# Kernel tuning notes

Hardware: AMD Instinct MI355X
Metric: run time of the kernel (lower is better)

The kernel has to match this reference:

```python
import jax, jax.numpy as jnp
import numpy as np

B, T, K = 256, 512, 128          # batch, seq_len, n_tag
START, STOP = 126, 127           # tag2idx[START_TAG], tag2idx[STOP_TAG]
NEG = -10000.0                   # same constant the torch module uses


def setup_inputs() -> dict:
    key = jax.random.key(0)
    k1, k2, k3 = jax.random.split(key, 3)
    feats = jax.random.normal(k1, (B, T, K), dtype=jnp.float32)
    tags = jax.random.randint(k2, (B, T), 0, 126)  # never START/STOP
    # learned CRF transition matrix: trans[to, from]
    transitions = 0.1 * jax.random.normal(k3, (K, K), dtype=jnp.float32)
    transitions = transitions.at[START, :].set(NEG).at[:, STOP].set(NEG)
    return {"feats": feats, "tags": tags, "transitions": transitions}


def _forward_alg(feats, trans):
    """Batched CRF forward algorithm. feats [B,T,K] -> log Z [B]."""
    b = feats.shape[0]
    init = jnp.full((b, K), NEG, feats.dtype).at[:, START].set(0.0)

    def step(alpha, feat_t):
        # scores[b, to, from] = alpha[b, from] + trans[to, from]
        scores = alpha[:, None, :] + trans[None, :, :]
        alpha_new = jax.nn.logsumexp(scores, axis=-1) + feat_t
        return alpha_new, None

    alpha, _ = jax.lax.scan(step, init, jnp.swapaxes(feats, 0, 1))
    return jax.nn.logsumexp(alpha + trans[STOP][None, :], axis=-1)


def _score_sentence(feats, tags, trans):
    """Batched gold path score. feats [B,T,K], tags [B,T] -> [B]."""
    b = feats.shape[0]
    start_col = jnp.full((b, 1), START, tags.dtype)
    tags_ext = jnp.concatenate([start_col, tags], axis=1)      # [B,T+1]
    trans_sc = trans[tags_ext[:, 1:], tags_ext[:, :-1]].sum(axis=1)
    emit_sc = jnp.take_along_axis(feats, tags[..., None], axis=2)[..., 0].sum(axis=1)
    return trans_sc + emit_sc + trans[STOP, tags[:, -1]]


def _viterbi(feats, trans):
    """Batched Viterbi decode. Returns (path_score [B], path [B,T])."""
    b = feats.shape[0]
    init = jnp.full((b, K), NEG, feats.dtype).at[:, START].set(0.0)

    def step(alpha, feat_t):
        scores = alpha[:, None, :] + trans[None, :, :]   # [B,to,from]
        bptr = jnp.argmax(scores, axis=-1)               # [B,to]
        alpha_new = jnp.max(scores, axis=-1) + feat_t
        return alpha_new, bptr

    alpha, bptrs = jax.lax.scan(step, init, jnp.swapaxes(feats, 0, 1))
    term = alpha + trans[STOP][None, :]
    last_tag = jnp.argmax(term, axis=-1)                 # [B]
    path_score = jnp.max(term, axis=-1)

    def back(tag_t, bp_t):
        prev = jnp.take_along_axis(bp_t, tag_t[:, None], axis=1)[:, 0]
        return prev, tag_t

    _, path = jax.lax.scan(back, last_tag, bptrs, reverse=True)  # [T,B]
    return path_score, jnp.swapaxes(path, 0, 1)


def reference(feats, tags, transitions):
    log_z = _forward_alg(feats, transitions)             # forward_alg per sentence
    gold = _score_sentence(feats, tags, transitions)     # score_sentence
    path_score, pred = _viterbi(feats, transitions)      # viterbi_decode
    loss = jnp.sum(log_z - gold) / jnp.float32(feats.shape[0] * feats.shape[1])
    return loss, path_score, pred
```

## Files before the change

kernel.cpp:

```cpp
#include <hip/hip_runtime.h>
#include <cstdint>
#include <cstddef>

#define BB 256
#define TT 512
#define KK 128
#define START_TAG 126
#define STOP_TAG 127
#define NEGV (-10000.0f)
#define NINF (-__builtin_huge_valf())

template<int CTRL>
__device__ __forceinline__ float dppf(float v, float old) {
  return __int_as_float(__builtin_amdgcn_update_dpp(
      __float_as_int(old), __float_as_int(v), CTRL, 0xf, 0xf, false));
}
template<int CTRL>
__device__ __forceinline__ int dppi(int v, int old) {
  return __builtin_amdgcn_update_dpp(old, v, CTRL, 0xf, 0xf, false);
}
__device__ __forceinline__ float wave_max63(float x) {
  x = fmaxf(x, dppf<0x111>(x, NINF));
  x = fmaxf(x, dppf<0x112>(x, NINF));
  x = fmaxf(x, dppf<0x114>(x, NINF));
  x = fmaxf(x, dppf<0x118>(x, NINF));
  x = fmaxf(x, dppf<0x142>(x, NINF));
  x = fmaxf(x, dppf<0x143>(x, NINF));
  return x;
}
__device__ __forceinline__ float max3f(float a, float b, float c) {
  float d;
  asm("v_max3_f32 %0, %1, %2, %3" : "=v"(d) : "v"(a), "v"(b), "v"(c));
  return d;
}
__device__ __forceinline__ int paddr(int i) { return (i >> 5) * 36 + (i & 31); }

__global__ __launch_bounds__(256, 1) void crf256(
    const float* __restrict__ feats, const float* __restrict__ trans,
    const int* __restrict__ tags,
    float* __restrict__ pscore, int* __restrict__ lasttag,
    float* __restrict__ alphaS, float* __restrict__ gb)
{
  const int bid = blockIdx.x;
  const bool isv = bid < BB;
  const int b = isv ? bid : bid - BB;
  const int tid = threadIdx.x;
  const int to = tid >> 1;
  const int h  = tid & 1;
  const int lane = tid & 63;
  const int wv = tid >> 6;

  __shared__ __align__(16) float BUF[2][144];
  __shared__ __align__(16) float pwm[4];
  __shared__ float vitm[2]; __shared__ int viti[2];
  __shared__ float reds[2]; __shared__ float redg[4];

  float R[64];
  {
    const float4* tr = (const float4*)(trans + (size_t)to * KK + h * 64);
#pragma unroll
    for (int c = 0; c < 16; ++c) {
      float4 v = tr[c];
      if (isv) { R[4*c+0]=v.x; R[4*c+1]=v.y; R[4*c+2]=v.z; R[4*c+3]=v.w; }
      else     { R[4*c+0]=__expf(v.x); R[4*c+1]=__expf(v.y);
                 R[4*c+2]=__expf(v.z); R[4*c+3]=__expf(v.w); }
    }
  }

  if (h == 0) BUF[0][paddr(to)] = isv ? ((to==START_TAG)?0.0f:NEGV)
                                      : ((to==START_TAG)?1.0f:0.0f);
  __syncthreads();

  const float* fb = feats + (size_t)b * TT * KK + to;
  float* aSb = alphaS + (size_t)b * TT * KK + to;

  float M = 0.0f;
  float fcur = fb[0];
  int cur = 0;

#pragma unroll 4
  for (int t = 0; t < TT; ++t) {
    const int tn = (t + 1 < TT) ? t + 1 : t;
    float fnext = fb[(size_t)tn * KK];
    const float* Bc = &BUF[cur][0];
    const int base = h * 72;

    if (isv) {
      float4 p = *(const float4*)&Bc[base];
      float m0 = fmaxf(p.x + R[0], p.y + R[1]);
      float m1 = fmaxf(p.z + R[2], p.w + R[3]);
#pragma unroll
      for (int c = 1; c < 16; ++c) {
        p = *(const float4*)&Bc[base + (c>>3)*36 + (c&7)*4];
        m0 = max3f(m0, p.x + R[4*c+0], p.y + R[4*c+1]);
        m1 = max3f(m1, p.z + R[4*c+2], p.w + R[4*c+3]);
      }
      float m = fmaxf(m0, m1);
      m = fmaxf(m, dppf<0xB1>(m, m));
      if (h == 0) {
        float a = m + fcur;
        BUF[cur ^ 1][paddr(to)] = a;
        aSb[(size_t)t * KK] = a;
      }
    } else {
      float corr = 1.0f;
      if ((t & 3) == 0 && t) {
        float4 w = *(const float4*)&pwm[0];
        float pmax = fmaxf(fmaxf(w.x, w.y), fmaxf(w.z, w.w));
        M += __logf(pmax);
        corr = 1.0f / pmax;
      }
      float s0=0.f, s1=0.f, s2=0.f, s3=0.f;
#pragma unroll
      for (int c = 0; c < 16; ++c) {
        float4 p = *(const float4*)&Bc[base + (c>>3)*36 + (c&7)*4];
        s0 = fmaf(R[4*c+0], p.x, s0);
        s1 = fmaf(R[4*c+1], p.y, s1);
        s2 = fmaf(R[4*c+2], p.z, s2);
        s3 = fmaf(R[4*c+3], p.w, s3);
      }
      float s = (s0 + s1) + (s2 + s3);
      s = s + dppf<0xB1>(s, s);
      float ef = __expf(fcur);
      if ((t & 3) == 0 && t) ef *= corr;
      float pv = s * ef;
      if (h == 0) BUF[cur ^ 1][paddr(to)] = pv;
      if ((t & 3) == 3) {
        float wm = wave_max63(pv);
        if (lane == 63) pwm[wv] = wm;
      }
    }
    __syncthreads();
    cur ^= 1;
    fcur = fnext;
  }

  if (isv) {
    if (tid < KK) {
      float term = BUF[cur][paddr(tid)] + trans[(size_t)STOP_TAG * KK + tid];
      float m = term; int i = tid;
#pragma unroll
      for (int off = 1; off < 64; off <<= 1) {
        float mo = __shfl_xor(m, off, 64);
        int   io = __shfl_xor(i, off, 64);
        if (mo > m || (mo == m && io < i)) { m = mo; i = io; }
      }
      if (lane == 0) { vitm[tid >> 6] = m; viti[tid >> 6] = i; }
    }
    __syncthreads();
    if (tid == 0) {
      float m = vitm[0]; int i = viti[0];
      if (vitm[1] > m || (vitm[1] == m && viti[1] < i)) { m = vitm[1]; i = viti[1]; }
      pscore[b] = m; lasttag[b] = i;
    }
  } else {
    if (tid < KK) {
      float e = BUF[cur][paddr(tid)] * __expf(trans[(size_t)STOP_TAG * KK + tid]);
#pragma unroll
      for (int off = 1; off < 64; off <<= 1) e += __shfl_xor(e, off, 64);
      if (lane == 0) reds[tid >> 6] = e;
    }
    const int* tg = tags + (size_t)b * TT;
    const float* fg = feats + (size_t)b * TT * KK;
    float g = 0.0f;
#pragma unroll
    for (int k2 = 0; k2 < 2; ++k2) {
      int t = tid + k2 * 256;
      int ct = tg[t];
      int pv2 = (t == 0) ? START_TAG : tg[t - 1];
      g += trans[(size_t)ct * KK + pv2] + fg[(size_t)t * KK + ct];
      if (t == TT - 1) g += trans[(size_t)STOP_TAG * KK + ct];
    }
#pragma unroll
    for (int off = 1; off < 64; off <<= 1) g += __shfl_xor(g, off, 64);
    if (lane == 0) redg[wv] = g;
    __syncthreads();
    if (tid == 0) {
      float sg = redg[0] + redg[1] + redg[2] + redg[3];
      gb[b] = (M + __logf(reds[0] + reds[1])) - sg;
    }
  }
}

__global__ __launch_bounds__(64) void backtrace_loss(
    const float* __restrict__ alphaS, const float* __restrict__ trans,
    const int* __restrict__ lasttag, const float* __restrict__ gb,
    float* __restrict__ pred, float* __restrict__ loss_out)
{
  const int lane = threadIdx.x;
  if (blockIdx.x == BB) {
    float v = gb[lane] + gb[lane + 64] + gb[lane + 128] + gb[lane + 192];
#pragma unroll
    for (int off = 1; off < 64; off <<= 1) v += __shfl_xor(v, off, 64);
    if (lane == 0) loss_out[0] = v / (float)(BB * TT);
    return;
  }
  const int b = blockIdx.x;
  __shared__ float tl[KK * KK];
  {
    const float4* src = (const float4*)trans;
    float4* dst = (float4*)tl;
#pragma unroll
    for (int i = 0; i < (KK * KK / 4) / 64; ++i) dst[lane + i * 64] = src[lane + i * 64];
  }
  int tag = lasttag[b];
  if (lane == 0) pred[(size_t)b * TT + (TT - 1)] = (float)tag;
  const float* arow = alphaS + (size_t)b * TT * KK;

  float p0[8], p1[8];
#pragma unroll
  for (int j = 0; j < 8; ++j) {
    int r = TT - 2 - j;
    p0[j] = arow[(size_t)r * KK + lane];
    p1[j] = arow[(size_t)r * KK + 64 + lane];
  }
  __syncthreads();

  for (int rb = TT - 2; rb >= 0; rb -= 8) {
#pragma unroll
    for (int j = 0; j < 8; ++j) {
      int r = rb - j;
      if (r >= 0) {
        float x0 = p0[j] + tl[tag * KK + lane];
        float x1 = p1[j] + tl[tag * KK + 64 + lane];
        float m = fmaxf(x0, x1);
        float M = wave_max63(m);
        M = __int_as_float(__builtin_amdgcn_readlane(__float_as_int(M), 63));
        unsigned long long b0 = __ballot(x0 == M);
        unsigned long long b1 = __ballot(x1 == M);
        tag = b0 ? (int)__builtin_ctzll(b0) : 64 + (int)__builtin_ctzll(b1);
        if (lane == 0) pred[(size_t)b * TT + r] = (float)tag;
        int rp = r - 8;
        if (rp >= 0) {
          p0[j] = arow[(size_t)rp * KK + lane];
          p1[j] = arow[(size_t)rp * KK + 64 + lane];
        }
      }
    }
  }
}

__global__ __launch_bounds__(768) void crf_main_fb(
    const float* __restrict__ feats, const float* __restrict__ trans,
    float* __restrict__ logz, float* __restrict__ pscore,
    int* __restrict__ lasttag, uint8_t* __restrict__ bptr)
{
  const int b = blockIdx.x;
  const int tid = threadIdx.x;
  const bool is_fwd = tid < 256;
  const int lane = tid & 63;

  __shared__ __align__(16) float P[2][144];
  __shared__ __align__(16) float AV[2][144];
  __shared__ __align__(16) float redmF[2][4];
  __shared__ float reds[4];
  __shared__ float vitm[8];
  __shared__ int   viti[8];

  int myto, h;
  if (is_fwd) { myto = tid >> 1; h = tid & 1; }
  else { int q = tid - 256; myto = q >> 2; h = q & 3; }

  float R[64];
  if (is_fwd) {
    const float4* tr = (const float4*)(trans + (size_t)myto * KK + h * 64);
#pragma unroll
    for (int c = 0; c < 16; ++c) {
      float4 v = tr[c];
      R[4*c+0]=expf(v.x); R[4*c+1]=expf(v.y); R[4*c+2]=expf(v.z); R[4*c+3]=expf(v.w);
    }
  } else {
    const float4* tr = (const float4*)(trans + (size_t)myto * KK + h * 32);
#pragma unroll
    for (int c = 0; c < 8; ++c) {
      float4 v = tr[c];
      R[4*c+0]=v.x; R[4*c+1]=v.y; R[4*c+2]=v.z; R[4*c+3]=v.w;
    }
  }

  if (is_fwd) { if (h == 0) P[0][paddr(myto)] = (myto==START_TAG)?1.0f:0.0f; }
  else        { if (h == 0) AV[0][paddr(myto)] = (myto==START_TAG)?0.0f:NEGV; }
  if (tid < 4) redmF[1][tid] = 0.0f;
  __syncthreads();

  const float* fb = feats + (size_t)b * TT * KK + myto;
  uint8_t* bp = bptr + (size_t)b * TT * KK + myto;

  float fcur = fb[0];
  float Mprev = 0.0f;
  float aCarry = 0.0f;
  int cur = 0;

  for (int t = 0; t < TT; ++t) {
    const int tn = (t + 1 < TT) ? t + 1 : t;
    float fnext = fb[(size_t)tn * KK];
    const int rd = (t + 1) & 1, wr = t & 1;

    if (is_fwd) {
      float4 rv = *(const float4*)&redmF[rd][0];
      float M1 = fmaxf(fmaxf(rv.x, rv.y), fmaxf(rv.z, rv.w));
      const float* Pc = &P[cur][0];
      const int base = h * 72;
      float s0=0.f, s1=0.f, s2=0.f, s3=0.f;
#pragma unroll
      for (int c = 0; c < 16; ++c) {
        float4 p = *(const float4*)&Pc[base + (c>>3)*36 + (c&7)*4];
        s0 = fmaf(R[4*c+0], p.x, s0);
        s1 = fmaf(R[4*c+1], p.y, s1);
        s2 = fmaf(R[4*c+2], p.z, s2);
        s3 = fmaf(R[4*c+3], p.w, s3);
      }
      float s = (s0 + s1) + (s2 + s3);
      s = s + dppf<0xB1>(s, s);
      float a = Mprev + logf(s) + fcur;
      float wm = wave_max63(a);
      if (lane == 63) redmF[wr][tid >> 6] = wm;
      float pv = expf(a - M1);
      if (h == 0) P[cur ^ 1][paddr(myto)] = pv;
      Mprev = M1;
      aCarry = a;
    } else {
      const float* Ac = &AV[cur][0];
      const int base = h * 36;
      const int fb0 = h * 32;
      float4 p0 = *(const float4*)&Ac[base];
      float m0 = p0.x + R[0], m1 = p0.y + R[1], m2 = p0.z + R[2], m3 = p0.w + R[3];
      int i0 = fb0, i1 = fb0+1, i2 = fb0+2, i3 = fb0+3;
#pragma unroll
      for (int c = 1; c < 8; ++c) {
        float4 p = *(const float4*)&Ac[base + c*4];
        float v0 = p.x + R[4*c+0]; if (v0 > m0) { m0 = v0; i0 = fb0+4*c+0; }
        float v1 = p.y + R[4*c+1]; if (v1 > m1) { m1 = v1; i1 = fb0+4*c+1; }
        float v2 = p.z + R[4*c+2]; if (v2 > m2) { m2 = v2; i2 = fb0+4*c+2; }
        float v3 = p.w + R[4*c+3]; if (v3 > m3) { m3 = v3; i3 = fb0+4*c+3; }
      }
      float m = m0; int i = i0;
      if (m1 > m || (m1 == m && i1 < i)) { m = m1; i = i1; }
      if (m2 > m || (m2 == m && i2 < i)) { m = m2; i = i2; }
      if (m3 > m || (m3 == m && i3 < i)) { m = m3; i = i3; }
      { float mo = dppf<0xB1>(m, m); int io = dppi<0xB1>(i, i);
        if (mo > m || (mo == m && io < i)) { m = mo; i = io; } }
      { float mo = dppf<0x4E>(m, m); int io = dppi<0x4E>(i, i);
        if (mo > m || (mo == m && io < i)) { m = mo; i = io; } }
      float a = m + fcur;
      if (h == 0) { AV[cur ^ 1][paddr(myto)] = a; bp[(size_t)t * KK] = (uint8_t)i; }
      aCarry = a;
    }
    __syncthreads();
    cur ^= 1;
    fcur = fnext;
  }

  float tstop = trans[(size_t)STOP_TAG * KK + myto];
  float term = aCarry + tstop;
  float M = 0.0f;
  if (is_fwd) {
    float wm = wave_max63(term);
    if (lane == 63) redmF[0][tid >> 6] = wm;
  } else {
    float m = term; int i = myto;
#pragma unroll
    for (int off = 1; off < 64; off <<= 1) {
      float mo = __shfl_xor(m, off, 64);
      int   io = __shfl_xor(i, off, 64);
      if (mo > m || (mo == m && io < i)) { m = mo; i = io; }
    }
    if (lane == 0) { vitm[(tid>>6)-4] = m; viti[(tid>>6)-4] = i; }
  }
  __syncthreads();
  if (is_fwd) {
    float4 rv = *(const float4*)&redmF[0][0];
    M = fmaxf(fmaxf(rv.x, rv.y), fmaxf(rv.z, rv.w));
    float e = (h == 0) ? expf(term - M) : 0.0f;
#pragma unroll
    for (int off = 1; off < 64; off <<= 1) e += __shfl_xor(e, off, 64);
    if (lane == 0) reds[tid >> 6] = e;
  } else if (tid == 256) {
    float m = vitm[0]; int i = viti[0];
#pragma unroll
    for (int w = 1; w < 8; ++w)
      if (vitm[w] > m || (vitm[w] == m && viti[w] < i)) { m = vitm[w]; i = viti[w]; }
    pscore[b] = m; lasttag[b] = i;
  }
  __syncthreads();
  if (tid == 0) logz[b] = M + logf(reds[0] + reds[1] + reds[2] + reds[3]);
}

__global__ __launch_bounds__(256) void backtrace_kernel(
    const uint8_t* __restrict__ bptr, const int* __restrict__ lasttag,
    float* __restrict__ pred)
{
  const int b = blockIdx.x;
  const int tid = threadIdx.x;
  __shared__ __align__(16) uint8_t lb[(TT / 2) * KK];
  __shared__ int tagcarry;
  if (tid == 0) tagcarry = lasttag[b];

  for (int half = 1; half >= 0; --half) {
    __syncthreads();
    const float4* src = reinterpret_cast<const float4*>(
        bptr + ((size_t)b * TT + (size_t)half * (TT / 2)) * KK);
    float4* dst = reinterpret_cast<float4*>(lb);
    for (int i = tid; i < (TT / 2) * KK / 16; i += 256) dst[i] = src[i];
    __syncthreads();
    if (tid == 0) {
      int tag = tagcarry;
      for (int t = TT / 2 - 1; t >= 0; --t) {
        int gt = half * (TT / 2) + t;
        pred[(size_t)b * TT + gt] = (float)tag;
        tag = lb[t * KK + tag];
      }
      tagcarry = tag;
    }
  }
}

__global__ __launch_bounds__(64) void gold_kernel(
    const float* __restrict__ feats, const int* __restrict__ tags,
    const float* __restrict__ trans, const float* __restrict__ logz,
    float* __restrict__ gb)
{
  const int b = blockIdx.x;
  const int lane = threadIdx.x;
  const int* tg = tags + (size_t)b * TT;
  const float* fb = feats + (size_t)b * TT * KK;
  float g = 0.0f;
#pragma unroll
  for (int k = 0; k < TT / 64; ++k) {
    int t = lane * (TT / 64) + k;
    int ct = tg[t];
    int pv = (t == 0) ? START_TAG : tg[t - 1];
    g += trans[ct * KK + pv] + fb[(size_t)t * KK + ct];
  }
  if (lane == 63) g += trans[STOP_TAG * KK + tg[TT - 1]];
#pragma unroll
  for (int off = 1; off <= 32; off <<= 1) g += __shfl_xor(g, off, 64);
  if (lane == 0) gb[b] = logz[b] - g;
}

__global__ __launch_bounds__(256) void loss_reduce(
    const float* __restrict__ gb, float* __restrict__ out)
{
  const int tid = threadIdx.x;
  const int lane = tid & 63, wv = tid >> 6;
  float v = gb[tid];
#pragma unroll
  for (int off = 1; off <= 32; off <<= 1) v += __shfl_xor(v, off, 64);
  __shared__ float red[4];
  if (lane == 0) red[wv] = v;
  __syncthreads();
  if (tid == 0) out[0] = (red[0] + red[1] + red[2] + red[3]) / (float)(BB * TT);
}

extern "C" void kernel_launch(void* const* d_in, const int* in_sizes, int n_in,
                              void* d_out, int out_size, void* d_ws, size_t ws_size,
                              hipStream_t stream) {
  const float* feats = (const float*)d_in[0];
  const int*   tags  = (const int*)d_in[1];
  const float* trans = (const float*)d_in[2];

  float* out    = (float*)d_out;
  float* loss   = out;
  float* pscore = out + 1;
  float* pred   = out + 1 + BB;
  (void)in_sizes; (void)n_in; (void)out_size;

  const size_t alpha_bytes = (size_t)BB * TT * KK * sizeof(float);
  const bool cheap = ws_size >= alpha_bytes + 4096;

  if (cheap) {
    float* alphaS  = (float*)d_ws;
    char*  wsend   = (char*)d_ws + alpha_bytes;
    int*   lasttag = (int*)(wsend);
    float* gb      = (float*)(wsend + BB * sizeof(int));
    crf256<<<2 * BB, 256, 0, stream>>>(feats, trans, tags, pscore, lasttag,
                                       alphaS, gb);
    backtrace_loss<<<BB + 1, 64, 0, stream>>>(alphaS, trans, lasttag, gb,
                                              pred, loss);
  } else {
    uint8_t* bptr    = (uint8_t*)d_ws;
    char*    wsend   = (char*)d_ws + (size_t)BB * TT * KK;
    float*   logz    = (float*)(wsend);
    int*     lasttag = (int*)(wsend + BB * sizeof(float));
    float*   gb      = (float*)(wsend + BB * sizeof(float) + BB * sizeof(int));
    crf_main_fb<<<BB, 768, 0, stream>>>(feats, trans, logz, pscore, lasttag, bptr);
    backtrace_kernel<<<BB, 256, 0, stream>>>(bptr, lasttag, pred);
    gold_kernel<<<BB, 64, 0, stream>>>(feats, tags, trans, logz, gb);
    loss_reduce<<<1, 256, 0, stream>>>(gb, loss);
  }
}
```

Measured before the change: 348.4 us.

## Split each tag's reduction across 8 lanes with 1024-thread CRF blocks

Each sequence block grows from 256 to 1024 threads, so every destination tag's 128-wide max or sum-product is split across 8 lanes of 16 elements instead of 2 lanes of 64. The shared alpha buffer gets a new padded layout, and the cross-lane combine adds DPP and shuffle steps. Per-step work on the serial recurrence is shorter and register pressure drops, but every time step now needs a block-wide barrier across 16 waves plus extra reduction steps.

```diff
diff --git a/kernel.cpp b/kernel.cpp
--- a/kernel.cpp
+++ b/kernel.cpp
@@ -33,9 +33,10 @@
   asm("v_max3_f32 %0, %1, %2, %3" : "=v"(d) : "v"(a), "v"(b), "v"(c));
   return d;
 }
+__device__ __forceinline__ int paddr20(int i) { return (i >> 4) * 20 + (i & 15); }
 __device__ __forceinline__ int paddr(int i) { return (i >> 5) * 36 + (i & 31); }
 
-__global__ __launch_bounds__(256, 1) void crf256(
+__global__ __launch_bounds__(1024, 8) void crf1k(
     const float* __restrict__ feats, const float* __restrict__ trans,
     const int* __restrict__ tags,
     float* __restrict__ pscore, int* __restrict__ lasttag,
@@ -45,21 +46,21 @@
   const bool isv = bid < BB;
   const int b = isv ? bid : bid - BB;
   const int tid = threadIdx.x;
-  const int to = tid >> 1;
-  const int h  = tid & 1;
+  const int to = tid >> 3;
+  const int h  = tid & 7;
   const int lane = tid & 63;
   const int wv = tid >> 6;
 
-  __shared__ __align__(16) float BUF[2][144];
-  __shared__ __align__(16) float pwm[4];
+  __shared__ __align__(16) float BUF[2][160];
+  __shared__ float pwm[16];
   __shared__ float vitm[2]; __shared__ int viti[2];
-  __shared__ float reds[2]; __shared__ float redg[4];
-
-  float R[64];
+  __shared__ float reds[2]; __shared__ float redg[8];
+
+  float R[16];
   {
-    const float4* tr = (const float4*)(trans + (size_t)to * KK + h * 64);
-#pragma unroll
-    for (int c = 0; c < 16; ++c) {
+    const float4* tr = (const float4*)(trans + (size_t)to * KK + h * 16);
+#pragma unroll
+    for (int c = 0; c < 4; ++c) {
       float4 v = tr[c];
       if (isv) { R[4*c+0]=v.x; R[4*c+1]=v.y; R[4*c+2]=v.z; R[4*c+3]=v.w; }
       else     { R[4*c+0]=__expf(v.x); R[4*c+1]=__expf(v.y);
@@ -67,8 +68,8 @@
     }
   }
 
-  if (h == 0) BUF[0][paddr(to)] = isv ? ((to==START_TAG)?0.0f:NEGV)
-                                      : ((to==START_TAG)?1.0f:0.0f);
+  if (h == 0) BUF[0][paddr20(to)] = isv ? ((to==START_TAG)?0.0f:NEGV)
+                                        : ((to==START_TAG)?1.0f:0.0f);
   __syncthreads();
 
   const float* fb = feats + (size_t)b * TT * KK + to;
@@ -78,53 +79,66 @@
   float fcur = fb[0];
   int cur = 0;
 
-#pragma unroll 4
   for (int t = 0; t < TT; ++t) {
     const int tn = (t + 1 < TT) ? t + 1 : t;
     float fnext = fb[(size_t)tn * KK];
-    const float* Bc = &BUF[cur][0];
-    const int base = h * 72;
+    const float* Bc = &BUF[cur][h * 20];
 
     if (isv) {
-      float4 p = *(const float4*)&Bc[base];
-      float m0 = fmaxf(p.x + R[0], p.y + R[1]);
-      float m1 = fmaxf(p.z + R[2], p.w + R[3]);
-#pragma unroll
-      for (int c = 1; c < 16; ++c) {
-        p = *(const float4*)&Bc[base + (c>>3)*36 + (c&7)*4];
-        m0 = max3f(m0, p.x + R[4*c+0], p.y + R[4*c+1]);
-        m1 = max3f(m1, p.z + R[4*c+2], p.w + R[4*c+3]);
-      }
-      float m = fmaxf(m0, m1);
+      float4 p0 = *(const float4*)&Bc[0];
+      float4 p1 = *(const float4*)&Bc[4];
+      float4 p2 = *(const float4*)&Bc[8];
+      float4 p3 = *(const float4*)&Bc[12];
+      float m = fmaxf(p0.x + R[0], p0.y + R[1]);
+      m = max3f(m, p0.z + R[2],  p0.w + R[3]);
+      m = max3f(m, p1.x + R[4],  p1.y + R[5]);
+      m = max3f(m, p1.z + R[6],  p1.w + R[7]);
+      m = max3f(m, p2.x + R[8],  p2.y + R[9]);
+      m = max3f(m, p2.z + R[10], p2.w + R[11]);
+      m = max3f(m, p3.x + R[12], p3.y + R[13]);
+      m = max3f(m, p3.z + R[14], p3.w + R[15]);
       m = fmaxf(m, dppf<0xB1>(m, m));
+      m = fmaxf(m, dppf<0x4E>(m, m));
+      m = fmaxf(m, __shfl_xor(m, 4, 64));
       if (h == 0) {
         float a = m + fcur;
-        BUF[cur ^ 1][paddr(to)] = a;
+        BUF[cur ^ 1][paddr20(to)] = a;
         aSb[(size_t)t * KK] = a;
       }
     } else {
       float corr = 1.0f;
       if ((t & 3) == 0 && t) {
-        float4 w = *(const float4*)&pwm[0];
-        float pmax = fmaxf(fmaxf(w.x, w.y), fmaxf(w.z, w.w));
+        float4 w0 = *(const float4*)&pwm[0];
+        float4 w1 = *(const float4*)&pwm[4];
+        float4 w2 = *(const float4*)&pwm[8];
+        float4 w3 = *(const float4*)&pwm[12];
+        float pmax = fmaxf(
+          fmaxf(fmaxf(fmaxf(w0.x,w0.y),fmaxf(w0.z,w0.w)),
+                fmaxf(fmaxf(w1.x,w1.y),fmaxf(w1.z,w1.w))),
+          fmaxf(fmaxf(fmaxf(w2.x,w2.y),fmaxf(w2.z,w2.w)),
+                fmaxf(fmaxf(w3.x,w3.y),fmaxf(w3.z,w3.w))));
         M += __logf(pmax);
         corr = 1.0f / pmax;
       }
-      float s0=0.f, s1=0.f, s2=0.f, s3=0.f;
-#pragma unroll
-      for (int c = 0; c < 16; ++c) {
-        float4 p = *(const float4*)&Bc[base + (c>>3)*36 + (c&7)*4];
-        s0 = fmaf(R[4*c+0], p.x, s0);
-        s1 = fmaf(R[4*c+1], p.y, s1);
-        s2 = fmaf(R[4*c+2], p.z, s2);
-        s3 = fmaf(R[4*c+3], p.w, s3);
-      }
+      float4 p0 = *(const float4*)&Bc[0];
+      float4 p1 = *(const float4*)&Bc[4];
+      float4 p2 = *(const float4*)&Bc[8];
+      float4 p3 = *(const float4*)&Bc[12];
+      float s0 = R[0]*p0.x, s1 = R[1]*p0.y, s2 = R[2]*p0.z, s3 = R[3]*p0.w;
+      s0 = fmaf(R[4],  p1.x, s0); s1 = fmaf(R[5],  p1.y, s1);
+      s2 = fmaf(R[6],  p1.z, s2); s3 = fmaf(R[7],  p1.w, s3);
+      s0 = fmaf(R[8],  p2.x, s0); s1 = fmaf(R[9],  p2.y, s1);
+      s2 = fmaf(R[10], p2.z, s2); s3 = fmaf(R[11], p2.w, s3);
+      s0 = fmaf(R[12], p3.x, s0); s1 = fmaf(R[13], p3.y, s1);
+      s2 = fmaf(R[14], p3.z, s2); s3 = fmaf(R[15], p3.w, s3);
       float s = (s0 + s1) + (s2 + s3);
       s = s + dppf<0xB1>(s, s);
+      s = s + dppf<0x4E>(s, s);
+      s = s + __shfl_xor(s, 4, 64);
       float ef = __expf(fcur);
       if ((t & 3) == 0 && t) ef *= corr;
       float pv = s * ef;
-      if (h == 0) BUF[cur ^ 1][paddr(to)] = pv;
+      if (h == 0) BUF[cur ^ 1][paddr20(to)] = pv;
       if ((t & 3) == 3) {
         float wm = wave_max63(pv);
         if (lane == 63) pwm[wv] = wm;
@@ -137,7 +151,7 @@
 
   if (isv) {
     if (tid < KK) {
-      float term = BUF[cur][paddr(tid)] + trans[(size_t)STOP_TAG * KK + tid];
+      float term = BUF[cur][paddr20(tid)] + trans[(size_t)STOP_TAG * KK + tid];
       float m = term; int i = tid;
 #pragma unroll
       for (int off = 1; off < 64; off <<= 1) {
@@ -155,28 +169,25 @@
     }
   } else {
     if (tid < KK) {
-      float e = BUF[cur][paddr(tid)] * __expf(trans[(size_t)STOP_TAG * KK + tid]);
+      float e = BUF[cur][paddr20(tid)] * __expf(trans[(size_t)STOP_TAG * KK + tid]);
 #pragma unroll
       for (int off = 1; off < 64; off <<= 1) e += __shfl_xor(e, off, 64);
       if (lane == 0) reds[tid >> 6] = e;
     }
-    const int* tg = tags + (size_t)b * TT;
-    const float* fg = feats + (size_t)b * TT * KK;
-    float g = 0.0f;
-#pragma unroll
-    for (int k2 = 0; k2 < 2; ++k2) {
-      int t = tid + k2 * 256;
-      int ct = tg[t];
-      int pv2 = (t == 0) ? START_TAG : tg[t - 1];
-      g += trans[(size_t)ct * KK + pv2] + fg[(size_t)t * KK + ct];
-      if (t == TT - 1) g += trans[(size_t)STOP_TAG * KK + ct];
-    }
-#pragma unroll
-    for (int off = 1; off < 64; off <<= 1) g += __shfl_xor(g, off, 64);
-    if (lane == 0) redg[wv] = g;
+    if (tid < TT) {
+      const int* tg = tags + (size_t)b * TT;
+      const float* fg = feats + (size_t)b * TT * KK;
+      int ct = tg[tid];
+      int pv2 = (tid == 0) ? START_TAG : tg[tid - 1];
+      float g = trans[(size_t)ct * KK + pv2] + fg[(size_t)tid * KK + ct];
+      if (tid == TT - 1) g += trans[(size_t)STOP_TAG * KK + ct];
+#pragma unroll
+      for (int off = 1; off < 64; off <<= 1) g += __shfl_xor(g, off, 64);
+      if (lane == 0) redg[wv] = g;
+    }
     __syncthreads();
     if (tid == 0) {
-      float sg = redg[0] + redg[1] + redg[2] + redg[3];
+      float sg = redg[0]+redg[1]+redg[2]+redg[3]+redg[4]+redg[5]+redg[6]+redg[7];
       gb[b] = (M + __logf(reds[0] + reds[1])) - sg;
     }
   }
@@ -473,7 +484,7 @@
     char*  wsend   = (char*)d_ws + alpha_bytes;
     int*   lasttag = (int*)(wsend);
     float* gb      = (float*)(wsend + BB * sizeof(int));
-    crf256<<<2 * BB, 256, 0, stream>>>(feats, trans, tags, pscore, lasttag,
+    crf1k<<<2 * BB, 1024, 0, stream>>>(feats, trans, tags, pscore, lasttag,
                                        alphaS, gb);
     backtrace_loss<<<BB + 1, 64, 0, stream>>>(alphaS, trans, lasttag, gb,
                                               pred, loss);
```

After: 448.1 us. +28.6%, slower.

## Move transition matrix to LDS and process two sequences per block

Applied to the files above, without the earlier changes.

Replaces the per-thread register copy of the transition row with a padded LDS copy of the whole matrix shared by 512 threads. Each block now advances two batch elements at once, four threads per output tag, so each transition value read from LDS serves both sequences. Grid size halves (256 blocks of 512 threads). The intent is to cut register pressure and the number of serial recurrence blocks, at the cost of extra LDS traffic per step and a wider cross-lane reduction.

```diff
diff --git a/kernel.cpp b/kernel.cpp
--- a/kernel.cpp
+++ b/kernel.cpp
@@ -34,150 +34,203 @@
   return d;
 }
 __device__ __forceinline__ int paddr(int i) { return (i >> 5) * 36 + (i & 31); }
-
-__global__ __launch_bounds__(256, 1) void crf256(
+__device__ __forceinline__ int permpos(int f) {
+  int j = f >> 2;
+  int q = (j & 7) * 4 + (j >> 3);
+  return q * 4 + (f & 3);
+}
+
+__global__ __launch_bounds__(512) void crf_lds(
     const float* __restrict__ feats, const float* __restrict__ trans,
     const int* __restrict__ tags,
     float* __restrict__ pscore, int* __restrict__ lasttag,
     float* __restrict__ alphaS, float* __restrict__ gb)
 {
   const int bid = blockIdx.x;
-  const bool isv = bid < BB;
-  const int b = isv ? bid : bid - BB;
+  const bool isv = bid < (BB / 2);
+  const int b0 = (isv ? bid : bid - BB / 2) * 2;
   const int tid = threadIdx.x;
-  const int to = tid >> 1;
-  const int h  = tid & 1;
+  const int to = tid >> 2;
+  const int h  = tid & 3;
   const int lane = tid & 63;
   const int wv = tid >> 6;
 
-  __shared__ __align__(16) float BUF[2][144];
-  __shared__ __align__(16) float pwm[4];
-  __shared__ float vitm[2]; __shared__ int viti[2];
-  __shared__ float reds[2]; __shared__ float redg[4];
-
-  float R[64];
+  __shared__ __align__(16) float tl[32 * 129 * 4];
+  __shared__ __align__(16) float av[2][2][KK];
+  __shared__ __align__(16) float pwm0[8], pwm1[8];
+  __shared__ float vitm[2][2]; __shared__ int viti[2][2];
+  __shared__ float reds[2][2]; __shared__ float redg[2][8];
+
+  float4* tl4 = (float4*)tl;
   {
-    const float4* tr = (const float4*)(trans + (size_t)to * KK + h * 64);
-#pragma unroll
-    for (int c = 0; c < 16; ++c) {
-      float4 v = tr[c];
-      if (isv) { R[4*c+0]=v.x; R[4*c+1]=v.y; R[4*c+2]=v.z; R[4*c+3]=v.w; }
-      else     { R[4*c+0]=__expf(v.x); R[4*c+1]=__expf(v.y);
-                 R[4*c+2]=__expf(v.z); R[4*c+3]=__expf(v.w); }
-    }
-  }
-
-  if (h == 0) BUF[0][paddr(to)] = isv ? ((to==START_TAG)?0.0f:NEGV)
-                                      : ((to==START_TAG)?1.0f:0.0f);
+    const float4* src = (const float4*)trans;
+#pragma unroll
+    for (int i = 0; i < 8; ++i) {
+      int idx = tid + i * 512;
+      float4 v = src[idx];
+      if (!isv) { v.x = __expf(v.x); v.y = __expf(v.y);
+                  v.z = __expf(v.z); v.w = __expf(v.w); }
+      int row = idx >> 5, chunk = idx & 31;
+      tl4[chunk * 129 + row] = v;
+    }
+  }
+  if (tid < 2 * KK) {
+    int g = tid >> 7, f = tid & 127;
+    av[0][g][permpos(f)] = isv ? ((f == START_TAG) ? 0.0f : NEGV)
+                               : ((f == START_TAG) ? 1.0f : 0.0f);
+  }
   __syncthreads();
 
-  const float* fb = feats + (size_t)b * TT * KK + to;
-  float* aSb = alphaS + (size_t)b * TT * KK + to;
-
-  float M = 0.0f;
-  float fcur = fb[0];
+  const float* fbs0 = feats + (size_t)(b0 + 0) * TT * KK + to;
+  const float* fbs1 = feats + (size_t)(b0 + 1) * TT * KK + to;
+  float* aS0 = alphaS + (size_t)(b0 + 0) * TT * KK + to;
+  float* aS1 = alphaS + (size_t)(b0 + 1) * TT * KK + to;
+
+  float M0 = 0.0f, M1 = 0.0f;
+  float f0 = fbs0[0], f1 = fbs1[0];
+  const int wpos = permpos(to);
+  const int tbase = h * 8 * 129 + to;
   int cur = 0;
 
-#pragma unroll 4
   for (int t = 0; t < TT; ++t) {
     const int tn = (t + 1 < TT) ? t + 1 : t;
-    float fnext = fb[(size_t)tn * KK];
-    const float* Bc = &BUF[cur][0];
-    const int base = h * 72;
+    float f0n = fbs0[(size_t)tn * KK];
+    float f1n = fbs1[(size_t)tn * KK];
+    const float4* A0 = (const float4*)av[cur][0];
+    const float4* A1 = (const float4*)av[cur][1];
 
     if (isv) {
-      float4 p = *(const float4*)&Bc[base];
-      float m0 = fmaxf(p.x + R[0], p.y + R[1]);
-      float m1 = fmaxf(p.z + R[2], p.w + R[3]);
-#pragma unroll
-      for (int c = 1; c < 16; ++c) {
-        p = *(const float4*)&Bc[base + (c>>3)*36 + (c&7)*4];
-        m0 = max3f(m0, p.x + R[4*c+0], p.y + R[4*c+1]);
-        m1 = max3f(m1, p.z + R[4*c+2], p.w + R[4*c+3]);
-      }
-      float m = fmaxf(m0, m1);
-      m = fmaxf(m, dppf<0xB1>(m, m));
+      float m0, m1;
+      {
+        float4 tv = tl4[tbase];
+        float4 p = A0[h];
+        m0 = fmaxf(fmaxf(p.x + tv.x, p.y + tv.y), fmaxf(p.z + tv.z, p.w + tv.w));
+        float4 q = A1[h];
+        m1 = fmaxf(fmaxf(q.x + tv.x, q.y + tv.y), fmaxf(q.z + tv.z, q.w + tv.w));
+      }
+#pragma unroll
+      for (int c = 1; c < 8; ++c) {
+        float4 tv = tl4[tbase + c * 129];
+        float4 p = A0[c * 4 + h];
+        m0 = max3f(m0, p.x + tv.x, p.y + tv.y);
+        m0 = max3f(m0, p.z + tv.z, p.w + tv.w);
+        float4 q = A1[c * 4 + h];
+        m1 = max3f(m1, q.x + tv.x, q.y + tv.y);
+        m1 = max3f(m1, q.z + tv.z, q.w + tv.w);
+      }
+      m0 = fmaxf(m0, dppf<0xB1>(m0, m0));
+      m0 = fmaxf(m0, dppf<0x4E>(m0, m0));
+      m1 = fmaxf(m1, dppf<0xB1>(m1, m1));
+      m1 = fmaxf(m1, dppf<0x4E>(m1, m1));
       if (h == 0) {
-        float a = m + fcur;
-        BUF[cur ^ 1][paddr(to)] = a;
-        aSb[(size_t)t * KK] = a;
+        float a0 = m0 + f0, a1 = m1 + f1;
+        av[cur ^ 1][0][wpos] = a0;
+        av[cur ^ 1][1][wpos] = a1;
+        aS0[(size_t)t * KK] = a0;
+        aS1[(size_t)t * KK] = a1;
       }
     } else {
-      float corr = 1.0f;
+      float c0 = 1.0f, c1 = 1.0f;
       if ((t & 3) == 0 && t) {
-        float4 w = *(const float4*)&pwm[0];
-        float pmax = fmaxf(fmaxf(w.x, w.y), fmaxf(w.z, w.w));
-        M += __logf(pmax);
-        corr = 1.0f / pmax;
-      }
-      float s0=0.f, s1=0.f, s2=0.f, s3=0.f;
-#pragma unroll
-      for (int c = 0; c < 16; ++c) {
-        float4 p = *(const float4*)&Bc[base + (c>>3)*36 + (c&7)*4];
-        s0 = fmaf(R[4*c+0], p.x, s0);
-        s1 = fmaf(R[4*c+1], p.y, s1);
-        s2 = fmaf(R[4*c+2], p.z, s2);
-        s3 = fmaf(R[4*c+3], p.w, s3);
-      }
-      float s = (s0 + s1) + (s2 + s3);
-      s = s + dppf<0xB1>(s, s);
-      float ef = __expf(fcur);
-      if ((t & 3) == 0 && t) ef *= corr;
-      float pv = s * ef;
-      if (h == 0) BUF[cur ^ 1][paddr(to)] = pv;
+        float4 w0 = *(const float4*)&pwm0[0];
+        float4 w1 = *(const float4*)&pwm0[4];
+        float pm0 = fmaxf(fmaxf(fmaxf(w0.x, w0.y), fmaxf(w0.z, w0.w)),
+                          fmaxf(fmaxf(w1.x, w1.y), fmaxf(w1.z, w1.w)));
+        float4 x0 = *(const float4*)&pwm1[0];
+        float4 x1 = *(const float4*)&pwm1[4];
+        float pm1 = fmaxf(fmaxf(fmaxf(x0.x, x0.y), fmaxf(x0.z, x0.w)),
+                          fmaxf(fmaxf(x1.x, x1.y), fmaxf(x1.z, x1.w)));
+        M0 += __logf(pm0); c0 = 1.0f / pm0;
+        M1 += __logf(pm1); c1 = 1.0f / pm1;
+      }
+      float sa = 0.f, sb = 0.f, ta = 0.f, tb = 0.f;
+#pragma unroll
+      for (int c = 0; c < 8; ++c) {
+        float4 tv = tl4[tbase + c * 129];
+        float4 p = A0[c * 4 + h];
+        sa = fmaf(tv.x, p.x, sa); sb = fmaf(tv.y, p.y, sb);
+        sa = fmaf(tv.z, p.z, sa); sb = fmaf(tv.w, p.w, sb);
+        float4 q = A1[c * 4 + h];
+        ta = fmaf(tv.x, q.x, ta); tb = fmaf(tv.y, q.y, tb);
+        ta = fmaf(tv.z, q.z, ta); tb = fmaf(tv.w, q.w, tb);
+      }
+      float s = sa + sb, u = ta + tb;
+      s = s + dppf<0xB1>(s, s); s = s + dppf<0x4E>(s, s);
+      u = u + dppf<0xB1>(u, u); u = u + dppf<0x4E>(u, u);
+      float e0 = __expf(f0), e1 = __expf(f1);
+      if ((t & 3) == 0 && t) { e0 *= c0; e1 *= c1; }
+      float pv0 = s * e0, pv1 = u * e1;
+      if (h == 0) {
+        av[cur ^ 1][0][wpos] = pv0;
+        av[cur ^ 1][1][wpos] = pv1;
+      }
       if ((t & 3) == 3) {
-        float wm = wave_max63(pv);
-        if (lane == 63) pwm[wv] = wm;
+        float wm0 = wave_max63(pv0);
+        float wm1 = wave_max63(pv1);
+        if (lane == 63) { pwm0[wv] = wm0; pwm1[wv] = wm1; }
       }
     }
     __syncthreads();
     cur ^= 1;
-    fcur = fnext;
+    f0 = f0n; f1 = f1n;
   }
 
   if (isv) {
     if (tid < KK) {
-      float term = BUF[cur][paddr(tid)] + trans[(size_t)STOP_TAG * KK + tid];
-      float m = term; int i = tid;
-#pragma unroll
-      for (int off = 1; off < 64; off <<= 1) {
-        float mo = __shfl_xor(m, off, 64);
-        int   io = __shfl_xor(i, off, 64);
-        if (mo > m || (mo == m && io < i)) { m = mo; i = io; }
-      }
-      if (lane == 0) { vitm[tid >> 6] = m; viti[tid >> 6] = i; }
+      const int f = tid;
+      float ts = trans[(size_t)STOP_TAG * KK + f];
+#pragma unroll
+      for (int g = 0; g < 2; ++g) {
+        float term = av[cur][g][permpos(f)] + ts;
+        float m = term; int i = f;
+#pragma unroll
+        for (int off = 1; off < 64; off <<= 1) {
+          float mo = __shfl_xor(m, off, 64);
+          int   io = __shfl_xor(i, off, 64);
+          if (mo > m || (mo == m && io < i)) { m = mo; i = io; }
+        }
+        if (lane == 0) { vitm[g][wv] = m; viti[g][wv] = i; }
+      }
     }
     __syncthreads();
-    if (tid == 0) {
-      float m = vitm[0]; int i = viti[0];
-      if (vitm[1] > m || (vitm[1] == m && viti[1] < i)) { m = vitm[1]; i = viti[1]; }
-      pscore[b] = m; lasttag[b] = i;
+    if (tid < 2) {
+      int g = tid;
+      float m = vitm[g][0]; int i = viti[g][0];
+      if (vitm[g][1] > m || (vitm[g][1] == m && viti[g][1] < i)) { m = vitm[g][1]; i = viti[g][1]; }
+      pscore[b0 + g] = m; lasttag[b0 + g] = i;
     }
   } else {
     if (tid < KK) {
-      float e = BUF[cur][paddr(tid)] * __expf(trans[(size_t)STOP_TAG * KK + tid]);
-#pragma unroll
-      for (int off = 1; off < 64; off <<= 1) e += __shfl_xor(e, off, 64);
-      if (lane == 0) reds[tid >> 6] = e;
-    }
-    const int* tg = tags + (size_t)b * TT;
-    const float* fg = feats + (size_t)b * TT * KK;
-    float g = 0.0f;
-#pragma unroll
-    for (int k2 = 0; k2 < 2; ++k2) {
-      int t = tid + k2 * 256;
-      int ct = tg[t];
-      int pv2 = (t == 0) ? START_TAG : tg[t - 1];
-      g += trans[(size_t)ct * KK + pv2] + fg[(size_t)t * KK + ct];
-      if (t == TT - 1) g += trans[(size_t)STOP_TAG * KK + ct];
-    }
-#pragma unroll
-    for (int off = 1; off < 64; off <<= 1) g += __shfl_xor(g, off, 64);
-    if (lane == 0) redg[wv] = g;
+      const int f = tid;
+      float es = __expf(trans[(size_t)STOP_TAG * KK + f]);
+#pragma unroll
+      for (int g = 0; g < 2; ++g) {
+        float e = av[cur][g][permpos(f)] * es;
+#pragma unroll
+        for (int off = 1; off < 64; off <<= 1) e += __shfl_xor(e, off, 64);
+        if (lane == 0) reds[g][wv] = e;
+      }
+    }
+#pragma unroll
+    for (int g = 0; g < 2; ++g) {
+      const int* tg = tags + (size_t)(b0 + g) * TT;
+      const float* fg = feats + (size_t)(b0 + g) * TT * KK;
+      int ct = tg[tid];
+      int pv2 = (tid == 0) ? START_TAG : tg[tid - 1];
+      float gl = trans[(size_t)ct * KK + pv2] + fg[(size_t)tid * KK + ct];
+      if (tid == TT - 1) gl += trans[(size_t)STOP_TAG * KK + ct];
+#pragma unroll
+      for (int off = 1; off < 64; off <<= 1) gl += __shfl_xor(gl, off, 64);
+      if (lane == 0) redg[g][wv] = gl;
+    }
     __syncthreads();
-    if (tid == 0) {
-      float sg = redg[0] + redg[1] + redg[2] + redg[3];
-      gb[b] = (M + __logf(reds[0] + reds[1])) - sg;
+    if (tid < 2) {
+      int g = tid;
+      float sg = 0.f;
+#pragma unroll
+      for (int w = 0; w < 8; ++w) sg += redg[g][w];
+      float Mg = g ? M1 : M0;
+      gb[b0 + g] = (Mg + __logf(reds[g][0] + reds[g][1])) - sg;
     }
   }
 }
@@ -473,8 +526,8 @@
     char*  wsend   = (char*)d_ws + alpha_bytes;
     int*   lasttag = (int*)(wsend);
     float* gb      = (float*)(wsend + BB * sizeof(int));
-    crf256<<<2 * BB, 256, 0, stream>>>(feats, trans, tags, pscore, lasttag,
-                                       alphaS, gb);
+    crf_lds<<<BB, 512, 0, stream>>>(feats, trans, tags, pscore, lasttag,
+                                    alphaS, gb);
     backtrace_loss<<<BB + 1, 64, 0, stream>>>(alphaS, trans, lasttag, gb,
                                               pred, loss);
   } else {
```

New measurement: 523.0 us. 1.5x slower.

## Split each CRF row across four lanes with 512-thread blocks

Applied to the files above, without the earlier changes.

The recurrence kernel now assigns four threads per output tag instead of two. Each thread keeps 32 transition values in named registers, pinned with empty asm, and the four partial max or sum results are combined with an extra DPP step. This halves the serial per-step dependency chain and register footprint, at the cost of more threads and wider intra-step reductions. The backtrace kernel also uses 256 threads to stage the transition matrix into shared memory, then leaves the serial traceback to a single wave.

```diff
diff --git a/kernel.cpp b/kernel.cpp
--- a/kernel.cpp
+++ b/kernel.cpp
@@ -35,7 +35,7 @@
 }
 __device__ __forceinline__ int paddr(int i) { return (i >> 5) * 36 + (i & 31); }
 
-__global__ __launch_bounds__(256, 1) void crf256(
+__global__ __launch_bounds__(512, 4) void crf512(
     const float* __restrict__ feats, const float* __restrict__ trans,
     const int* __restrict__ tags,
     float* __restrict__ pscore, int* __restrict__ lasttag,
@@ -45,25 +45,38 @@
   const bool isv = bid < BB;
   const int b = isv ? bid : bid - BB;
   const int tid = threadIdx.x;
-  const int to = tid >> 1;
-  const int h  = tid & 1;
+  const int to = tid >> 2;
+  const int h  = tid & 3;
   const int lane = tid & 63;
   const int wv = tid >> 6;
 
   __shared__ __align__(16) float BUF[2][144];
-  __shared__ __align__(16) float pwm[4];
+  __shared__ __align__(16) float pwm[8];
   __shared__ float vitm[2]; __shared__ int viti[2];
-  __shared__ float reds[2]; __shared__ float redg[4];
-
-  float R[64];
+  __shared__ float reds[2]; __shared__ float redg[8];
+
+  float r00,r01,r02,r03,r04,r05,r06,r07,r08,r09,r10,r11,r12,r13,r14,r15,
+        r16,r17,r18,r19,r20,r21,r22,r23,r24,r25,r26,r27,r28,r29,r30,r31;
   {
-    const float4* tr = (const float4*)(trans + (size_t)to * KK + h * 64);
-#pragma unroll
-    for (int c = 0; c < 16; ++c) {
-      float4 v = tr[c];
-      if (isv) { R[4*c+0]=v.x; R[4*c+1]=v.y; R[4*c+2]=v.z; R[4*c+3]=v.w; }
-      else     { R[4*c+0]=__expf(v.x); R[4*c+1]=__expf(v.y);
-                 R[4*c+2]=__expf(v.z); R[4*c+3]=__expf(v.w); }
+    const float4* tr = (const float4*)(trans + (size_t)to * KK + h * 32);
+    float4 v;
+    v = tr[0]; r00=v.x; r01=v.y; r02=v.z; r03=v.w;
+    v = tr[1]; r04=v.x; r05=v.y; r06=v.z; r07=v.w;
+    v = tr[2]; r08=v.x; r09=v.y; r10=v.z; r11=v.w;
+    v = tr[3]; r12=v.x; r13=v.y; r14=v.z; r15=v.w;
+    v = tr[4]; r16=v.x; r17=v.y; r18=v.z; r19=v.w;
+    v = tr[5]; r20=v.x; r21=v.y; r22=v.z; r23=v.w;
+    v = tr[6]; r24=v.x; r25=v.y; r26=v.z; r27=v.w;
+    v = tr[7]; r28=v.x; r29=v.y; r30=v.z; r31=v.w;
+    if (!isv) {
+      r00=__expf(r00); r01=__expf(r01); r02=__expf(r02); r03=__expf(r03);
+      r04=__expf(r04); r05=__expf(r05); r06=__expf(r06); r07=__expf(r07);
+      r08=__expf(r08); r09=__expf(r09); r10=__expf(r10); r11=__expf(r11);
+      r12=__expf(r12); r13=__expf(r13); r14=__expf(r14); r15=__expf(r15);
+      r16=__expf(r16); r17=__expf(r17); r18=__expf(r18); r19=__expf(r19);
+      r20=__expf(r20); r21=__expf(r21); r22=__expf(r22); r23=__expf(r23);
+      r24=__expf(r24); r25=__expf(r25); r26=__expf(r26); r27=__expf(r27);
+      r28=__expf(r28); r29=__expf(r29); r30=__expf(r30); r31=__expf(r31);
     }
   }
 
@@ -78,25 +91,47 @@
   float fcur = fb[0];
   int cur = 0;
 
-#pragma unroll 4
   for (int t = 0; t < TT; ++t) {
+    asm volatile("" : "+v"(r00),"+v"(r01),"+v"(r02),"+v"(r03),
+                      "+v"(r04),"+v"(r05),"+v"(r06),"+v"(r07));
+    asm volatile("" : "+v"(r08),"+v"(r09),"+v"(r10),"+v"(r11),
+                      "+v"(r12),"+v"(r13),"+v"(r14),"+v"(r15));
+    asm volatile("" : "+v"(r16),"+v"(r17),"+v"(r18),"+v"(r19),
+                      "+v"(r20),"+v"(r21),"+v"(r22),"+v"(r23));
+    asm volatile("" : "+v"(r24),"+v"(r25),"+v"(r26),"+v"(r27),
+                      "+v"(r28),"+v"(r29),"+v"(r30),"+v"(r31));
     const int tn = (t + 1 < TT) ? t + 1 : t;
     float fnext = fb[(size_t)tn * KK];
-    const float* Bc = &BUF[cur][0];
-    const int base = h * 72;
+    const float* Bc = &BUF[cur][h * 36];
 
     if (isv) {
-      float4 p = *(const float4*)&Bc[base];
-      float m0 = fmaxf(p.x + R[0], p.y + R[1]);
-      float m1 = fmaxf(p.z + R[2], p.w + R[3]);
-#pragma unroll
-      for (int c = 1; c < 16; ++c) {
-        p = *(const float4*)&Bc[base + (c>>3)*36 + (c&7)*4];
-        m0 = max3f(m0, p.x + R[4*c+0], p.y + R[4*c+1]);
-        m1 = max3f(m1, p.z + R[4*c+2], p.w + R[4*c+3]);
-      }
+      float4 p = *(const float4*)&Bc[0];
+      float m0 = fmaxf(p.x + r00, p.y + r01);
+      float m1 = fmaxf(p.z + r02, p.w + r03);
+      p = *(const float4*)&Bc[4];
+      m0 = max3f(m0, p.x + r04, p.y + r05);
+      m1 = max3f(m1, p.z + r06, p.w + r07);
+      p = *(const float4*)&Bc[8];
+      m0 = max3f(m0, p.x + r08, p.y + r09);
+      m1 = max3f(m1, p.z + r10, p.w + r11);
+      p = *(const float4*)&Bc[12];
+      m0 = max3f(m0, p.x + r12, p.y + r13);
+      m1 = max3f(m1, p.z + r14, p.w + r15);
+      p = *(const float4*)&Bc[16];
+      m0 = max3f(m0, p.x + r16, p.y + r17);
+      m1 = max3f(m1, p.z + r18, p.w + r19);
+      p = *(const float4*)&Bc[20];
+      m0 = max3f(m0, p.x + r20, p.y + r21);
+      m1 = max3f(m1, p.z + r22, p.w + r23);
+      p = *(const float4*)&Bc[24];
+      m0 = max3f(m0, p.x + r24, p.y + r25);
+      m1 = max3f(m1, p.z + r26, p.w + r27);
+      p = *(const float4*)&Bc[28];
+      m0 = max3f(m0, p.x + r28, p.y + r29);
+      m1 = max3f(m1, p.z + r30, p.w + r31);
       float m = fmaxf(m0, m1);
       m = fmaxf(m, dppf<0xB1>(m, m));
+      m = fmaxf(m, dppf<0x4E>(m, m));
       if (h == 0) {
         float a = m + fcur;
         BUF[cur ^ 1][paddr(to)] = a;
@@ -105,22 +140,39 @@
     } else {
       float corr = 1.0f;
       if ((t & 3) == 0 && t) {
-        float4 w = *(const float4*)&pwm[0];
-        float pmax = fmaxf(fmaxf(w.x, w.y), fmaxf(w.z, w.w));
+        float4 w0 = *(const float4*)&pwm[0];
+        float4 w1 = *(const float4*)&pwm[4];
+        float pmax = fmaxf(fmaxf(fmaxf(w0.x, w0.y), fmaxf(w0.z, w0.w)),
+                           fmaxf(fmaxf(w1.x, w1.y), fmaxf(w1.z, w1.w)));
         M += __logf(pmax);
         corr = 1.0f / pmax;
       }
-      float s0=0.f, s1=0.f, s2=0.f, s3=0.f;
-#pragma unroll
-      for (int c = 0; c < 16; ++c) {
-        float4 p = *(const float4*)&Bc[base + (c>>3)*36 + (c&7)*4];
-        s0 = fmaf(R[4*c+0], p.x, s0);
-        s1 = fmaf(R[4*c+1], p.y, s1);
-        s2 = fmaf(R[4*c+2], p.z, s2);
-        s3 = fmaf(R[4*c+3], p.w, s3);
-      }
+      float4 p = *(const float4*)&Bc[0];
+      float s0 = r00 * p.x, s1 = r01 * p.y, s2 = r02 * p.z, s3 = r03 * p.w;
+      p = *(const float4*)&Bc[4];
+      s0 = fmaf(r04, p.x, s0); s1 = fmaf(r05, p.y, s1);
+      s2 = fmaf(r06, p.z, s2); s3 = fmaf(r07, p.w, s3);
+      p = *(const float4*)&Bc[8];
+      s0 = fmaf(r08, p.x, s0); s1 = fmaf(r09, p.y, s1);
+      s2 = fmaf(r10, p.z, s2); s3 = fmaf(r11, p.w, s3);
+      p = *(const float4*)&Bc[12];
+      s0 = fmaf(r12, p.x, s0); s1 = fmaf(r13, p.y, s1);
+      s2 = fmaf(r14, p.z, s2); s3 = fmaf(r15, p.w, s3);
+      p = *(const float4*)&Bc[16];
+      s0 = fmaf(r16, p.x, s0); s1 = fmaf(r17, p.y, s1);
+      s2 = fmaf(r18, p.z, s2); s3 = fmaf(r19, p.w, s3);
+      p = *(const float4*)&Bc[20];
+      s0 = fmaf(r20, p.x, s0); s1 = fmaf(r21, p.y, s1);
+      s2 = fmaf(r22, p.z, s2); s3 = fmaf(r23, p.w, s3);
+      p = *(const float4*)&Bc[24];
+      s0 = fmaf(r24, p.x, s0); s1 = fmaf(r25, p.y, s1);
+      s2 = fmaf(r26, p.z, s2); s3 = fmaf(r27, p.w, s3);
+      p = *(const float4*)&Bc[28];
+      s0 = fmaf(r28, p.x, s0); s1 = fmaf(r29, p.y, s1);
+      s2 = fmaf(r30, p.z, s2); s3 = fmaf(r31, p.w, s3);
       float s = (s0 + s1) + (s2 + s3);
       s = s + dppf<0xB1>(s, s);
+      s = s + dppf<0x4E>(s, s);
       float ef = __expf(fcur);
       if ((t & 3) == 0 && t) ef *= corr;
       float pv = s * ef;
@@ -160,39 +212,39 @@
       for (int off = 1; off < 64; off <<= 1) e += __shfl_xor(e, off, 64);
       if (lane == 0) reds[tid >> 6] = e;
     }
-    const int* tg = tags + (size_t)b * TT;
-    const float* fg = feats + (size_t)b * TT * KK;
-    float g = 0.0f;
-#pragma unroll
-    for (int k2 = 0; k2 < 2; ++k2) {
-      int t = tid + k2 * 256;
-      int ct = tg[t];
-      int pv2 = (t == 0) ? START_TAG : tg[t - 1];
-      g += trans[(size_t)ct * KK + pv2] + fg[(size_t)t * KK + ct];
-      if (t == TT - 1) g += trans[(size_t)STOP_TAG * KK + ct];
-    }
-#pragma unroll
-    for (int off = 1; off < 64; off <<= 1) g += __shfl_xor(g, off, 64);
-    if (lane == 0) redg[wv] = g;
+    {
+      const int* tg = tags + (size_t)b * TT;
+      const float* fg = feats + (size_t)b * TT * KK;
+      int ct = tg[tid];
+      int pv2 = (tid == 0) ? START_TAG : tg[tid - 1];
+      float g = trans[(size_t)ct * KK + pv2] + fg[(size_t)tid * KK + ct];
+      if (tid == TT - 1) g += trans[(size_t)STOP_TAG * KK + ct];
+#pragma unroll
+      for (int off = 1; off < 64; off <<= 1) g += __shfl_xor(g, off, 64);
+      if (lane == 0) redg[wv] = g;
+    }
     __syncthreads();
     if (tid == 0) {
-      float sg = redg[0] + redg[1] + redg[2] + redg[3];
+      float sg = redg[0]+redg[1]+redg[2]+redg[3]+redg[4]+redg[5]+redg[6]+redg[7];
       gb[b] = (M + __logf(reds[0] + reds[1])) - sg;
     }
   }
 }
 
-__global__ __launch_bounds__(64) void backtrace_loss(
+__global__ __launch_bounds__(256) void backtrace_loss(
     const float* __restrict__ alphaS, const float* __restrict__ trans,
     const int* __restrict__ lasttag, const float* __restrict__ gb,
     float* __restrict__ pred, float* __restrict__ loss_out)
 {
-  const int lane = threadIdx.x;
+  const int tid = threadIdx.x;
+  const int lane = tid & 63;
   if (blockIdx.x == BB) {
-    float v = gb[lane] + gb[lane + 64] + gb[lane + 128] + gb[lane + 192];
-#pragma unroll
-    for (int off = 1; off < 64; off <<= 1) v += __shfl_xor(v, off, 64);
-    if (lane == 0) loss_out[0] = v / (float)(BB * TT);
+    if (tid < 64) {
+      float v = gb[lane] + gb[lane + 64] + gb[lane + 128] + gb[lane + 192];
+#pragma unroll
+      for (int off = 1; off < 64; off <<= 1) v += __shfl_xor(v, off, 64);
+      if (lane == 0) loss_out[0] = v / (float)(BB * TT);
+    }
     return;
   }
   const int b = blockIdx.x;
@@ -201,20 +253,23 @@
     const float4* src = (const float4*)trans;
     float4* dst = (float4*)tl;
 #pragma unroll
-    for (int i = 0; i < (KK * KK / 4) / 64; ++i) dst[lane + i * 64] = src[lane + i * 64];
-  }
+    for (int i = 0; i < (KK * KK / 4) / 256; ++i) dst[tid + i * 256] = src[tid + i * 256];
+  }
+  const float* arow = alphaS + (size_t)b * TT * KK;
+  float p0[8], p1[8];
+  if (tid < 64) {
+#pragma unroll
+    for (int j = 0; j < 8; ++j) {
+      int r = TT - 2 - j;
+      p0[j] = arow[(size_t)r * KK + lane];
+      p1[j] = arow[(size_t)r * KK + 64 + lane];
+    }
+  }
+  __syncthreads();
+  if (tid >= 64) return;
+
   int tag = lasttag[b];
   if (lane == 0) pred[(size_t)b * TT + (TT - 1)] = (float)tag;
-  const float* arow = alphaS + (size_t)b * TT * KK;
-
-  float p0[8], p1[8];
-#pragma unroll
-  for (int j = 0; j < 8; ++j) {
-    int r = TT - 2 - j;
-    p0[j] = arow[(size_t)r * KK + lane];
-    p1[j] = arow[(size_t)r * KK + 64 + lane];
-  }
-  __syncthreads();
 
   for (int rb = TT - 2; rb >= 0; rb -= 8) {
 #pragma unroll
@@ -473,10 +528,10 @@
     char*  wsend   = (char*)d_ws + alpha_bytes;
     int*   lasttag = (int*)(wsend);
     float* gb      = (float*)(wsend + BB * sizeof(int));
-    crf256<<<2 * BB, 256, 0, stream>>>(feats, trans, tags, pscore, lasttag,
+    crf512<<<2 * BB, 512, 0, stream>>>(feats, trans, tags, pscore, lasttag,
                                        alphaS, gb);
-    backtrace_loss<<<BB + 1, 64, 0, stream>>>(alphaS, trans, lasttag, gb,
-                                              pred, loss);
+    backtrace_loss<<<BB + 1, 256, 0, stream>>>(alphaS, trans, lasttag, gb,
+                                               pred, loss);
   } else {
     uint8_t* bptr    = (uint8_t*)d_ws;
     char*    wsend   = (char*)d_ws + (size_t)BB * TT * KK;
```

After: 361.1 us. 1.04x slower.
